# Kernel optimization log

Measured on AMD Instinct MI355X. Metric: run time of the kernel, lower is better.

## Reference

```python
import jax, jax.numpy as jnp
import numpy as np

QMIN, QMAX = -128, 127


def setup_inputs() -> dict:
    key = jax.random.key(0)
    kx, kw, kb = jax.random.split(key, 3)
    B, S, IN, OUT = 4, 2048, 4096, 4096
    x = jax.random.normal(kx, (B, S, IN), dtype=jnp.float32)
    # int8-valued weight stored as int32 for portability
    weight_int = jax.random.randint(kw, (OUT, IN), QMIN, QMAX + 1, dtype=jnp.int32)
    bias = jax.random.normal(kb, (OUT,), dtype=jnp.float32) * 0.02
    # plausible frozen qparams: x~N(0,1) -> range ~[-4,4]; weight range ~[-3,3] pre-quant
    scale_a = jnp.asarray(8.0 / 255.0, dtype=jnp.float32)
    zp_a = jnp.asarray(0, dtype=jnp.int32)
    weight_scale = jnp.asarray(6.0 / 255.0, dtype=jnp.float32)
    weight_zero_point = jnp.asarray(0, dtype=jnp.int32)
    return {
        "x": x,
        "weight_int": weight_int,
        "bias": bias,
        "scale_a": scale_a,
        "zp_a": zp_a,
        "weight_scale": weight_scale,
        "weight_zero_point": weight_zero_point,
    }


def reference(x, weight_int, bias, scale_a, zp_a, weight_scale, weight_zero_point):
    # fake-quantize activations: round(x/scale)+zp, clamp to int8 range
    zp_a_f = zp_a.astype(jnp.float32)
    x_int8 = jnp.clip(jnp.round(x / scale_a) + zp_a_f, QMIN, QMAX)
    x_cent = x_int8 - zp_a_f                                   # [B,S,IN]
    w_cent = weight_int.astype(jnp.float32) - weight_zero_point.astype(jnp.float32)  # [OUT,IN]
    y = jnp.einsum("bsi,oi->bso", x_cent, w_cent)              # dequant-space GEMM
    y = y * (scale_a * weight_scale)
    y = y + bias
    return y
```

## Files before the change

### kernel.cpp

```cpp
#include <hip/hip_runtime.h>
#include <stdint.h>

typedef int v4i  __attribute__((ext_vector_type(4)));
typedef int v16i __attribute__((ext_vector_type(16)));

__global__ void quant_x_kernel(const float* __restrict__ x,
                               int8_t* __restrict__ xq,
                               int* __restrict__ sum_x,
                               const float* __restrict__ p_scale,
                               const int* __restrict__ p_zp,
                               int K) {
    const int row = blockIdx.x;
    const int t = threadIdx.x;
    const float s = p_scale[0];
    const float zpf = (float)p_zp[0];
    const float* xr = x + (size_t)row * K;
    int8_t* qr = xq + (size_t)row * K;
    int lsum = 0;
    const int nchunk = K >> 10;
    for (int i = 0; i < nchunk; ++i) {
        const int idx = (i << 10) + (t << 2);
        const float4 v = *reinterpret_cast<const float4*>(xr + idx);
        const float f0 = fminf(fmaxf(rintf(v.x / s) + zpf, -128.f), 127.f);
        const float f1 = fminf(fmaxf(rintf(v.y / s) + zpf, -128.f), 127.f);
        const float f2 = fminf(fmaxf(rintf(v.z / s) + zpf, -128.f), 127.f);
        const float f3 = fminf(fmaxf(rintf(v.w / s) + zpf, -128.f), 127.f);
        const int i0 = (int)f0, i1 = (int)f1, i2 = (int)f2, i3 = (int)f3;
        lsum += i0 + i1 + i2 + i3;
        const unsigned pk = (unsigned)(i0 & 255) | ((unsigned)(i1 & 255) << 8) |
                            ((unsigned)(i2 & 255) << 16) | ((unsigned)(i3 & 255) << 24);
        *reinterpret_cast<unsigned*>(qr + idx) = pk;
    }
    __shared__ int wsum[4];
    #pragma unroll
    for (int off = 32; off > 0; off >>= 1) lsum += __shfl_down(lsum, off);
    if ((t & 63) == 0) wsum[t >> 6] = lsum;
    __syncthreads();
    if (t == 0) sum_x[row] = wsum[0] + wsum[1] + wsum[2] + wsum[3];
}

__global__ void quant_w_kernel(const int* __restrict__ w,
                               int8_t* __restrict__ wq,
                               int* __restrict__ sum_w,
                               int K) {
    const int row = blockIdx.x;
    const int t = threadIdx.x;
    const int* wr_ = w + (size_t)row * K;
    int8_t* qr = wq + (size_t)row * K;
    int lsum = 0;
    const int nchunk = K >> 10;
    for (int i = 0; i < nchunk; ++i) {
        const int idx = (i << 10) + (t << 2);
        const int4 v = *reinterpret_cast<const int4*>(wr_ + idx);
        lsum += v.x + v.y + v.z + v.w;
        const unsigned pk = (unsigned)(v.x & 255) | ((unsigned)(v.y & 255) << 8) |
                            ((unsigned)(v.z & 255) << 16) | ((unsigned)(v.w & 255) << 24);
        *reinterpret_cast<unsigned*>(qr + idx) = pk;
    }
    __shared__ int wsum[4];
    #pragma unroll
    for (int off = 32; off > 0; off >>= 1) lsum += __shfl_down(lsum, off);
    if ((t & 63) == 0) wsum[t >> 6] = lsum;
    __syncthreads();
    if (t == 0) sum_w[row] = wsum[0] + wsum[1] + wsum[2] + wsum[3];
}

#define BM 256
#define BN 256
#define BKB 64
#define NSLOT 4

__device__ __forceinline__ void gload_lds16(const void* g, void* l) {
    __builtin_amdgcn_global_load_lds(
        (const __attribute__((address_space(1))) unsigned int*)g,
        (__attribute__((address_space(3))) unsigned int*)l, 16, 0, 0);
}

#define MFMA_I8 __builtin_amdgcn_mfma_i32_32x32x32_i8

__global__ __launch_bounds__(512, 2)
void gemm_i8_kernel(const int8_t* __restrict__ xq,
                    const int8_t* __restrict__ wq,
                    const int* __restrict__ sum_x,
                    const int* __restrict__ sum_w,
                    const float* __restrict__ bias,
                    float* __restrict__ out,
                    const float* __restrict__ p_sa,
                    const int* __restrict__ p_zpa,
                    const float* __restrict__ p_sw,
                    const int* __restrict__ p_wzp,
                    int M, int N, int K) {
    __shared__ v4i ldsA[NSLOT][1024];
    __shared__ v4i ldsB[NSLOT][1024];

    const int tid = threadIdx.x;
    const int lane = tid & 63;
    const int wid = tid >> 6;
    const int wr = wid >> 2;
    const int wc = wid & 3;
    const int m0 = blockIdx.y * BM;
    const int n0 = blockIdx.x * BN;

    const int srow = tid >> 2;
    const int schunk = (tid & 3) ^ ((srow >> 1) & 3);
    const int8_t* aS = xq + (size_t)(m0 + srow) * K + schunk * 16;
    const int8_t* bS = wq + (size_t)(n0 + srow) * K + schunk * 16;
    const size_t half = (size_t)128 * K;
    const int dbase = wid * 64;

    const int sel = (lane >> 1) & 3;
    const int hi = lane >> 5;
    const int abase = (wr * 128 + (lane & 31)) * 4;
    const int bbase = (wc * 64 + (lane & 31)) * 4;
    const int c0 = hi ^ sel;
    const int c1 = (2 + hi) ^ sel;

    v16i acc[4][2] = {};
    v4i fb[2][4];
    v4i fa[2][8];

    const int NT = K / BKB;

    gload_lds16(aS,             &ldsA[0][dbase]);
    gload_lds16(aS + half,      &ldsA[0][dbase + 512]);
    gload_lds16(bS,             &ldsB[0][dbase]);
    gload_lds16(bS + half,      &ldsB[0][dbase + 512]);
    gload_lds16(aS + 64,        &ldsA[1][dbase]);
    gload_lds16(aS + half + 64, &ldsA[1][dbase + 512]);
    gload_lds16(bS + 64,        &ldsB[1][dbase]);
    gload_lds16(bS + half + 64, &ldsB[1][dbase + 512]);
    asm volatile("s_waitcnt vmcnt(4)" ::: "memory");
    __builtin_amdgcn_s_barrier();
    {
        const v4i* LA = ldsA[0];
        const v4i* LB = ldsB[0];
        fb[0][0] = LB[bbase + c0];        fb[0][1] = LB[bbase + c1];
        fb[0][2] = LB[bbase + 128 + c0];  fb[0][3] = LB[bbase + 128 + c1];
        fa[0][0] = LA[abase + c0];        fa[0][1] = LA[abase + c1];
        fa[0][2] = LA[abase + 128 + c0];  fa[0][3] = LA[abase + 128 + c1];
        fa[0][4] = LA[abase + 256 + c0];  fa[0][5] = LA[abase + 256 + c1];
        fa[0][6] = LA[abase + 384 + c0];  fa[0][7] = LA[abase + 384 + c1];
    }

#define ITER(PH, T_) do {                                                     \
        const int t_ = (T_);                                                  \
        if (t_ + 2 < NT) {                                                    \
            const int ns = (t_ + 2) & 3;                                      \
            const int8_t* pA = aS + (size_t)(t_ + 2) * BKB;                   \
            const int8_t* pB = bS + (size_t)(t_ + 2) * BKB;                   \
            gload_lds16(pA,        &ldsA[ns][dbase]);                         \
            gload_lds16(pA + half, &ldsA[ns][dbase + 512]);                   \
            gload_lds16(pB,        &ldsB[ns][dbase]);                         \
            gload_lds16(pB + half, &ldsB[ns][dbase + 512]);                   \
            asm volatile("s_waitcnt vmcnt(4)" ::: "memory");                  \
        } else if (t_ + 1 < NT) {                                             \
            asm volatile("s_waitcnt vmcnt(0)" ::: "memory");                  \
        }                                                                     \
        if (t_ + 1 < NT) {                                                    \
            const v4i* LA = ldsA[(t_ + 1) & 3];                               \
            const v4i* LB = ldsB[(t_ + 1) & 3];                               \
            fb[PH ^ 1][0] = LB[bbase + c0];                                   \
            fb[PH ^ 1][1] = LB[bbase + c1];                                   \
            fb[PH ^ 1][2] = LB[bbase + 128 + c0];                             \
            fb[PH ^ 1][3] = LB[bbase + 128 + c1];                             \
            fa[PH ^ 1][0] = LA[abase + c0];                                   \
            fa[PH ^ 1][1] = LA[abase + c1];                                   \
            fa[PH ^ 1][2] = LA[abase + 128 + c0];                             \
            fa[PH ^ 1][3] = LA[abase + 128 + c1];                             \
            fa[PH ^ 1][4] = LA[abase + 256 + c0];                             \
            fa[PH ^ 1][5] = LA[abase + 256 + c1];                             \
            fa[PH ^ 1][6] = LA[abase + 384 + c0];                             \
            fa[PH ^ 1][7] = LA[abase + 384 + c1];                             \
        }                                                                     \
        __builtin_amdgcn_s_setprio(1);                                        \
        acc[0][0] = MFMA_I8(fa[PH][0], fb[PH][0], acc[0][0], 0, 0, 0);        \
        acc[0][1] = MFMA_I8(fa[PH][0], fb[PH][2], acc[0][1], 0, 0, 0);        \
        acc[1][0] = MFMA_I8(fa[PH][2], fb[PH][0], acc[1][0], 0, 0, 0);        \
        acc[1][1] = MFMA_I8(fa[PH][2], fb[PH][2], acc[1][1], 0, 0, 0);        \
        acc[2][0] = MFMA_I8(fa[PH][4], fb[PH][0], acc[2][0], 0, 0, 0);        \
        acc[2][1] = MFMA_I8(fa[PH][4], fb[PH][2], acc[2][1], 0, 0, 0);        \
        acc[3][0] = MFMA_I8(fa[PH][6], fb[PH][0], acc[3][0], 0, 0, 0);        \
        acc[3][1] = MFMA_I8(fa[PH][6], fb[PH][2], acc[3][1], 0, 0, 0);        \
        acc[0][0] = MFMA_I8(fa[PH][1], fb[PH][1], acc[0][0], 0, 0, 0);        \
        acc[0][1] = MFMA_I8(fa[PH][1], fb[PH][3], acc[0][1], 0, 0, 0);        \
        acc[1][0] = MFMA_I8(fa[PH][3], fb[PH][1], acc[1][0], 0, 0, 0);        \
        acc[1][1] = MFMA_I8(fa[PH][3], fb[PH][3], acc[1][1], 0, 0, 0);        \
        acc[2][0] = MFMA_I8(fa[PH][5], fb[PH][1], acc[2][0], 0, 0, 0);        \
        acc[2][1] = MFMA_I8(fa[PH][5], fb[PH][3], acc[2][1], 0, 0, 0);        \
        acc[3][0] = MFMA_I8(fa[PH][7], fb[PH][1], acc[3][0], 0, 0, 0);        \
        acc[3][1] = MFMA_I8(fa[PH][7], fb[PH][3], acc[3][1], 0, 0, 0);        \
        __builtin_amdgcn_s_setprio(0);                                        \
        __builtin_amdgcn_s_barrier();                                         \
    } while (0)

    for (int tt = 0; tt < NT; tt += 2) {
        ITER(0, tt);
        ITER(1, tt + 1);
    }
#undef ITER

    const float stot = p_sa[0] * p_sw[0];
    const int zpa = p_zpa[0];
    const int wzp = p_wzp[0];
    const int kzz = K * zpa * wzp;
    const int coll = lane & 31;
    const int rhi = (lane >> 5) * 4;

    #pragma unroll
    for (int cf = 0; cf < 2; ++cf) {
        const int cg = n0 + wc * 64 + cf * 32 + coll;
        const int sw = sum_w[cg];
        const float bb = bias[cg];
        #pragma unroll
        for (int rf = 0; rf < 4; ++rf) {
            const int rbase = m0 + wr * 128 + rf * 32 + rhi;
            #pragma unroll
            for (int r = 0; r < 16; ++r) {
                const int rowg = rbase + (r & 3) + 8 * (r >> 2);
                const int iv = acc[rf][cf][r] - wzp * sum_x[rowg] - zpa * sw + kzz;
                out[(size_t)rowg * N + cg] = (float)iv * stot + bb;
            }
        }
    }
}

extern "C" void kernel_launch(void* const* d_in, const int* in_sizes, int n_in,
                              void* d_out, int out_size, void* d_ws, size_t ws_size,
                              hipStream_t stream) {
    const float* x     = (const float*)d_in[0];
    const int*   w     = (const int*)d_in[1];
    const float* bias  = (const float*)d_in[2];
    const float* p_sa  = (const float*)d_in[3];
    const int*   p_zpa = (const int*)d_in[4];
    const float* p_sw  = (const float*)d_in[5];
    const int*   p_wzp = (const int*)d_in[6];

    const int N = in_sizes[2];
    const int K = in_sizes[1] / N;
    const int M = in_sizes[0] / K;

    int8_t* xq = (int8_t*)d_ws;
    int8_t* wq = xq + (size_t)M * K;
    int* sum_x = (int*)(wq + (size_t)N * K);
    int* sum_w = sum_x + M;

    quant_x_kernel<<<M, 256, 0, stream>>>(x, xq, sum_x, p_sa, p_zpa, K);
    quant_w_kernel<<<N, 256, 0, stream>>>(w, wq, sum_w, K);

    dim3 grid(N / BN, M / BM);
    gemm_i8_kernel<<<grid, 512, 0, stream>>>(xq, wq, sum_x, sum_w, bias,
                                             (float*)d_out, p_sa, p_zpa, p_sw, p_wzp,
                                             M, N, K);
}
```

Baseline: 256.3 us.

## Load B fragments directly from global to registers, drop B LDS staging, remap blocks to XCDs

The weight operand is now read straight from global memory into registers with a one-tile register double buffer, so the B shared-memory buffer and its LDS reads go away. Only A is staged through LDS. The A swizzle is changed to reduce bank conflicts, and each tile's MFMA work is split into two halves separated by extra barriers. The 2D grid becomes a 1D grid with a block-id remap that spreads consecutive blocks across the 8 XCDs for L2 locality. In exchange, B is no longer shared through LDS across the two wave rows, so each B element is fetched from global memory by more waves, and the extra barriers plus the full vmcnt(0) wait every tile may serialize the loop.

Result: slower. 326.3 us (+27.3%).

```diff
diff --git a/kernel.cpp b/kernel.cpp
--- a/kernel.cpp
+++ b/kernel.cpp
@@ -91,113 +91,112 @@
                     const int* __restrict__ p_wzp,
                     int M, int N, int K) {
     __shared__ v4i ldsA[NSLOT][1024];
-    __shared__ v4i ldsB[NSLOT][1024];
 
     const int tid = threadIdx.x;
     const int lane = tid & 63;
     const int wid = tid >> 6;
     const int wr = wid >> 2;
     const int wc = wid & 3;
-    const int m0 = blockIdx.y * BM;
-    const int n0 = blockIdx.x * BN;
+
+    const int nwgy = M / BM;
+    const int nwg = nwgy * (N / BN);
+    const int bid = blockIdx.x;
+    const int v = (bid & 7) * (nwg >> 3) + (bid >> 3);
+    const int m0 = (v % nwgy) * BM;
+    const int n0 = (v / nwgy) * BN;
 
     const int srow = tid >> 2;
-    const int schunk = (tid & 3) ^ ((srow >> 1) & 3);
+    const int schunk = (tid & 3) ^ (((srow >> 1) ^ (srow >> 3)) & 3);
     const int8_t* aS = xq + (size_t)(m0 + srow) * K + schunk * 16;
-    const int8_t* bS = wq + (size_t)(n0 + srow) * K + schunk * 16;
     const size_t half = (size_t)128 * K;
     const int dbase = wid * 64;
 
-    const int sel = (lane >> 1) & 3;
+    const int sel = ((lane >> 1) ^ (lane >> 3)) & 3;
     const int hi = lane >> 5;
     const int abase = (wr * 128 + (lane & 31)) * 4;
-    const int bbase = (wc * 64 + (lane & 31)) * 4;
-    const int c0 = hi ^ sel;
-    const int c1 = (2 + hi) ^ sel;
+    const int c00 = hi ^ sel;
+    const int c01 = (2 + hi) ^ sel;
+
+    const int8_t* bP = wq + (size_t)(n0 + wc * 64 + (lane & 31)) * K + ((lane >> 5) << 4);
+    const size_t bcf = (size_t)32 * K;
 
     v16i acc[4][2] = {};
-    v4i fb[2][4];
-    v4i fa[2][8];
+    v4i bfA[4], bfB[4];
 
     const int NT = K / BKB;
 
     gload_lds16(aS,             &ldsA[0][dbase]);
     gload_lds16(aS + half,      &ldsA[0][dbase + 512]);
-    gload_lds16(bS,             &ldsB[0][dbase]);
-    gload_lds16(bS + half,      &ldsB[0][dbase + 512]);
     gload_lds16(aS + 64,        &ldsA[1][dbase]);
     gload_lds16(aS + half + 64, &ldsA[1][dbase + 512]);
-    gload_lds16(bS + 64,        &ldsB[1][dbase]);
-    gload_lds16(bS + half + 64, &ldsB[1][dbase + 512]);
-    asm volatile("s_waitcnt vmcnt(4)" ::: "memory");
+    bfA[0] = *reinterpret_cast<const v4i*>(bP);
+    bfA[1] = *reinterpret_cast<const v4i*>(bP + 32);
+    bfA[2] = *reinterpret_cast<const v4i*>(bP + bcf);
+    bfA[3] = *reinterpret_cast<const v4i*>(bP + bcf + 32);
+    asm volatile("s_waitcnt vmcnt(0)" ::: "memory");
+    __builtin_amdgcn_sched_barrier(0);
     __builtin_amdgcn_s_barrier();
-    {
-        const v4i* LA = ldsA[0];
-        const v4i* LB = ldsB[0];
-        fb[0][0] = LB[bbase + c0];        fb[0][1] = LB[bbase + c1];
-        fb[0][2] = LB[bbase + 128 + c0];  fb[0][3] = LB[bbase + 128 + c1];
-        fa[0][0] = LA[abase + c0];        fa[0][1] = LA[abase + c1];
-        fa[0][2] = LA[abase + 128 + c0];  fa[0][3] = LA[abase + 128 + c1];
-        fa[0][4] = LA[abase + 256 + c0];  fa[0][5] = LA[abase + 256 + c1];
-        fa[0][6] = LA[abase + 384 + c0];  fa[0][7] = LA[abase + 384 + c1];
-    }
-
-#define ITER(PH, T_) do {                                                     \
+
+#define TILE(BCUR, BNXT, T_) do {                                             \
         const int t_ = (T_);                                                  \
+        const v4i* LA = ldsA[t_ & 3];                                         \
+        \
+        const v4i a00 = LA[abase + c00];                                      \
+        const v4i a01 = LA[abase + c01];                                      \
+        const v4i a10 = LA[abase + 128 + c00];                                \
+        const v4i a11 = LA[abase + 128 + c01];                                \
         if (t_ + 2 < NT) {                                                    \
             const int ns = (t_ + 2) & 3;                                      \
-            const int8_t* pA = aS + (size_t)(t_ + 2) * BKB;                   \
-            const int8_t* pB = bS + (size_t)(t_ + 2) * BKB;                   \
-            gload_lds16(pA,        &ldsA[ns][dbase]);                         \
-            gload_lds16(pA + half, &ldsA[ns][dbase + 512]);                   \
-            gload_lds16(pB,        &ldsB[ns][dbase]);                         \
-            gload_lds16(pB + half, &ldsB[ns][dbase + 512]);                   \
-            asm volatile("s_waitcnt vmcnt(4)" ::: "memory");                  \
-        } else if (t_ + 1 < NT) {                                             \
-            asm volatile("s_waitcnt vmcnt(0)" ::: "memory");                  \
+            const int8_t* p = aS + (size_t)(t_ + 2) * BKB;                    \
+            gload_lds16(p,        &ldsA[ns][dbase]);                          \
+            gload_lds16(p + half, &ldsA[ns][dbase + 512]);                    \
         }                                                                     \
+        __builtin_amdgcn_s_barrier();                                         \
+        __builtin_amdgcn_s_setprio(1);                                        \
+        acc[0][0] = MFMA_I8(a00, BCUR[0], acc[0][0], 0, 0, 0);                \
+        acc[0][1] = MFMA_I8(a00, BCUR[2], acc[0][1], 0, 0, 0);                \
+        acc[1][0] = MFMA_I8(a10, BCUR[0], acc[1][0], 0, 0, 0);                \
+        acc[1][1] = MFMA_I8(a10, BCUR[2], acc[1][1], 0, 0, 0);                \
+        acc[0][0] = MFMA_I8(a01, BCUR[1], acc[0][0], 0, 0, 0);                \
+        acc[0][1] = MFMA_I8(a01, BCUR[3], acc[0][1], 0, 0, 0);                \
+        acc[1][0] = MFMA_I8(a11, BCUR[1], acc[1][0], 0, 0, 0);                \
+        acc[1][1] = MFMA_I8(a11, BCUR[3], acc[1][1], 0, 0, 0);                \
+        __builtin_amdgcn_s_setprio(0);                                        \
+        __builtin_amdgcn_s_barrier();                                         \
+        \
+        const v4i a20 = LA[abase + 256 + c00];                                \
+        const v4i a21 = LA[abase + 256 + c01];                                \
+        const v4i a30 = LA[abase + 384 + c00];                                \
+        const v4i a31 = LA[abase + 384 + c01];                                \
         if (t_ + 1 < NT) {                                                    \
-            const v4i* LA = ldsA[(t_ + 1) & 3];                               \
-            const v4i* LB = ldsB[(t_ + 1) & 3];                               \
-            fb[PH ^ 1][0] = LB[bbase + c0];                                   \
-            fb[PH ^ 1][1] = LB[bbase + c1];                                   \
-            fb[PH ^ 1][2] = LB[bbase + 128 + c0];                             \
-            fb[PH ^ 1][3] = LB[bbase + 128 + c1];                             \
-            fa[PH ^ 1][0] = LA[abase + c0];                                   \
-            fa[PH ^ 1][1] = LA[abase + c1];                                   \
-            fa[PH ^ 1][2] = LA[abase + 128 + c0];                             \
-            fa[PH ^ 1][3] = LA[abase + 128 + c1];                             \
-            fa[PH ^ 1][4] = LA[abase + 256 + c0];                             \
-            fa[PH ^ 1][5] = LA[abase + 256 + c1];                             \
-            fa[PH ^ 1][6] = LA[abase + 384 + c0];                             \
-            fa[PH ^ 1][7] = LA[abase + 384 + c1];                             \
+            const int8_t* q = bP + (size_t)(t_ + 1) * BKB;                    \
+            BNXT[0] = *reinterpret_cast<const v4i*>(q);                       \
+            BNXT[1] = *reinterpret_cast<const v4i*>(q + 32);                  \
+            BNXT[2] = *reinterpret_cast<const v4i*>(q + bcf);                 \
+            BNXT[3] = *reinterpret_cast<const v4i*>(q + bcf + 32);            \
         }                                                                     \
+        __builtin_amdgcn_s_barrier();                                         \
         __builtin_amdgcn_s_setprio(1);                                        \
-        acc[0][0] = MFMA_I8(fa[PH][0], fb[PH][0], acc[0][0], 0, 0, 0);        \
-        acc[0][1] = MFMA_I8(fa[PH][0], fb[PH][2], acc[0][1], 0, 0, 0);        \
-        acc[1][0] = MFMA_I8(fa[PH][2], fb[PH][0], acc[1][0], 0, 0, 0);        \
-        acc[1][1] = MFMA_I8(fa[PH][2], fb[PH][2], acc[1][1], 0, 0, 0);        \
-        acc[2][0] = MFMA_I8(fa[PH][4], fb[PH][0], acc[2][0], 0, 0, 0);        \
-        acc[2][1] = MFMA_I8(fa[PH][4], fb[PH][2], acc[2][1], 0, 0, 0);        \
-        acc[3][0] = MFMA_I8(fa[PH][6], fb[PH][0], acc[3][0], 0, 0, 0);        \
-        acc[3][1] = MFMA_I8(fa[PH][6], fb[PH][2], acc[3][1], 0, 0, 0);        \
-        acc[0][0] = MFMA_I8(fa[PH][1], fb[PH][1], acc[0][0], 0, 0, 0);        \
-        acc[0][1] = MFMA_I8(fa[PH][1], fb[PH][3], acc[0][1], 0, 0, 0);        \
-        acc[1][0] = MFMA_I8(fa[PH][3], fb[PH][1], acc[1][0], 0, 0, 0);        \
-        acc[1][1] = MFMA_I8(fa[PH][3], fb[PH][3], acc[1][1], 0, 0, 0);        \
-        acc[2][0] = MFMA_I8(fa[PH][5], fb[PH][1], acc[2][0], 0, 0, 0);        \
-        acc[2][1] = MFMA_I8(fa[PH][5], fb[PH][3], acc[2][1], 0, 0, 0);        \
-        acc[3][0] = MFMA_I8(fa[PH][7], fb[PH][1], acc[3][0], 0, 0, 0);        \
-        acc[3][1] = MFMA_I8(fa[PH][7], fb[PH][3], acc[3][1], 0, 0, 0);        \
+        acc[2][0] = MFMA_I8(a20, BCUR[0], acc[2][0], 0, 0, 0);                \
+        acc[2][1] = MFMA_I8(a20, BCUR[2], acc[2][1], 0, 0, 0);                \
+        acc[3][0] = MFMA_I8(a30, BCUR[0], acc[3][0], 0, 0, 0);                \
+        acc[3][1] = MFMA_I8(a30, BCUR[2], acc[3][1], 0, 0, 0);                \
+        acc[2][0] = MFMA_I8(a21, BCUR[1], acc[2][0], 0, 0, 0);                \
+        acc[2][1] = MFMA_I8(a21, BCUR[3], acc[2][1], 0, 0, 0);                \
+        acc[3][0] = MFMA_I8(a31, BCUR[1], acc[3][0], 0, 0, 0);                \
+        acc[3][1] = MFMA_I8(a31, BCUR[3], acc[3][1], 0, 0, 0);                \
         __builtin_amdgcn_s_setprio(0);                                        \
+           \
+        asm volatile("s_waitcnt vmcnt(0)" ::: "memory");                      \
+        __builtin_amdgcn_sched_barrier(0);                                    \
         __builtin_amdgcn_s_barrier();                                         \
     } while (0)
 
     for (int tt = 0; tt < NT; tt += 2) {
-        ITER(0, tt);
-        ITER(1, tt + 1);
-    }
-#undef ITER
+        TILE(bfA, bfB, tt);
+        TILE(bfB, bfA, tt + 1);
+    }
+#undef TILE
 
     const float stot = p_sa[0] * p_sw[0];
     const int zpa = p_zpa[0];
@@ -247,8 +246,8 @@
     quant_x_kernel<<<M, 256, 0, stream>>>(x, xq, sum_x, p_sa, p_zpa, K);
     quant_w_kernel<<<N, 256, 0, stream>>>(w, wq, sum_w, K);
 
-    dim3 grid(N / BN, M / BM);
-    gemm_i8_kernel<<<grid, 512, 0, stream>>>(xq, wq, sum_x, sum_w, bias,
-                                             (float*)d_out, p_sa, p_zpa, p_sw, p_wzp,
-                                             M, N, K);
-}
+    const int nwg = (M / BM) * (N / BN);
+    gemm_i8_kernel<<<nwg, 512, 0, stream>>>(xq, wq, sum_x, sum_w, bias,
+                                            (float*)d_out, p_sa, p_zpa, p_sw, p_wzp,
+                                            M, N, K);
+}
```
